# Optimization experiments

Hardware: AMD Instinct MI355X
Metric: run time of the kernel (lower is better)

The kernel has to match this reference:

```python
import jax, jax.numpy as jnp
import numpy as np

N, E = 40000, 640000
IN_DIM, EDGE_DIM, HID, H1 = 5, 11, 128, 4
NEG_SLOPE = 0.2


def _add_self_loops(ei, ea, n):
    # PyG GATConv default: add_self_loops=True, fill_value='mean' for edge_attr
    loop = jnp.arange(n, dtype=ei.dtype)
    ei2 = jnp.concatenate([ei, jnp.stack([loop, loop])], axis=1)
    ea2 = jnp.concatenate([ea, jnp.broadcast_to(ea.mean(0), (n, ea.shape[1]))], axis=0)
    return ei2, ea2


def _gat(x, ei, ea, W, We, a_src, a_dst, a_edge, b, H, C):
    # Single GATConv layer (eval mode, dropout inactive)
    n = x.shape[0]
    xh = (x @ W).reshape(n, H, C)            # [N,H,C]
    eh = (ea @ We).reshape(-1, H, C)         # [E,H,C]
    src, dst = ei[0], ei[1]
    a_s = (xh * a_src).sum(-1)               # [N,H]
    a_d = (xh * a_dst).sum(-1)               # [N,H]
    alpha = jax.nn.leaky_relu(a_s[src] + a_d[dst] + (eh * a_edge).sum(-1), NEG_SLOPE)  # [E,H]
    amax = jax.ops.segment_max(alpha, dst, num_segments=n)
    ex = jnp.exp(alpha - amax[dst])
    den = jax.ops.segment_sum(ex, dst, num_segments=n)
    w = ex / (den[dst] + 1e-16)              # softmax over inbound edges per dst
    out = jax.ops.segment_sum(xh[src] * w[:, :, None], dst, num_segments=n)  # [N,H,C]
    return out.reshape(n, H * C) + b


def setup_inputs() -> dict:
    key = jax.random.key(0)
    ks = jax.random.split(key, 20)
    s = 0.1
    return {
        "x": jax.random.normal(ks[0], (N, IN_DIM), jnp.float32),
        "edge_index": jax.random.randint(ks[1], (2, E), 0, N),
        "edge_attr": jax.random.normal(ks[2], (E, EDGE_DIM), jnp.float32),
        "W1": jax.random.normal(ks[3], (IN_DIM, H1 * HID), jnp.float32) * s,
        "We1": jax.random.normal(ks[4], (EDGE_DIM, H1 * HID), jnp.float32) * s,
        "a_src1": jax.random.normal(ks[5], (H1, HID), jnp.float32) * s,
        "a_dst1": jax.random.normal(ks[6], (H1, HID), jnp.float32) * s,
        "a_edge1": jax.random.normal(ks[7], (H1, HID), jnp.float32) * s,
        "b1": jnp.zeros((H1 * HID,), jnp.float32),
        # layer 2 (512 -> 128, 1 head)
        "W2": jax.random.normal(ks[8], (H1 * HID, HID), jnp.float32) * s,
        "We2": jax.random.normal(ks[9], (EDGE_DIM, HID), jnp.float32) * s,
        "a_src2": jax.random.normal(ks[10], (1, HID), jnp.float32) * s,
        "a_dst2": jax.random.normal(ks[11], (1, HID), jnp.float32) * s,
        "a_edge2": jax.random.normal(ks[12], (1, HID), jnp.float32) * s,
        "b2": jnp.zeros((HID,), jnp.float32),
        # final linear 128 -> 1
        "Wfc": jax.random.normal(ks[13], (HID, 1), jnp.float32) * s,
        "bfc": jnp.zeros((1,), jnp.float32),
    }


def reference(x, edge_index, edge_attr,
              W1, We1, a_src1, a_dst1, a_edge1, b1,
              W2, We2, a_src2, a_dst2, a_edge2, b2,
              Wfc, bfc):
    ei, ea = _add_self_loops(edge_index, edge_attr, x.shape[0])
    h = jax.nn.relu(_gat(x, ei, ea, W1, We1, a_src1, a_dst1, a_edge1, b1, H1, HID))
    h = jax.nn.relu(_gat(h, ei, ea, W2, We2, a_src2, a_dst2, a_edge2, b2, 1, HID))
    return jax.nn.sigmoid(h @ Wfc + bfc)
```

## Files before the change

### kernel.cpp

```cpp
#include <hip/hip_runtime.h>

#define NN   40000
#define EE   640000
#define IND  5
#define ED   11
#define HIDD 128
#define F1   512
#define PSB  2500

typedef unsigned short u16;
typedef unsigned int   u32;
typedef __attribute__((ext_vector_type(8))) short bf16x8;
typedef __attribute__((ext_vector_type(4))) float f32x4;

__device__ __forceinline__ float bf2f(u16 u) { return __uint_as_float(((u32)u) << 16); }
__device__ __forceinline__ u16 f2bf(float f) {
    u32 u = __float_as_uint(f);
    return (u16)((u + 0x7FFFu + ((u >> 16) & 1u)) >> 16);
}

__device__ __forceinline__ float wsum(float v) {
#pragma unroll
    for (int o = 32; o; o >>= 1) v += __shfl_xor(v, o, 64);
    return v;
}
__device__ __forceinline__ float lrelu(float v) { return v > 0.f ? v : 0.2f * v; }



#define SBLK 256
#define SGRID ((NN + SBLK - 1) / SBLK)
#define PREPG (SGRID + 33 + NN / 4)

__global__ void __launch_bounds__(256) k_prep(int* __restrict__ counts,
                                              float* __restrict__ consts,
                                              const float* __restrict__ We1,
                                              const float* __restrict__ ae1,
                                              const float* __restrict__ We2,
                                              const float* __restrict__ ae2,
                                              const float* __restrict__ W2,
                                              u16* __restrict__ bsw,
                                              const float* __restrict__ x,
                                              const float* __restrict__ W1,
                                              const float* __restrict__ as1,
                                              const float* __restrict__ ad1,
                                              float* __restrict__ aS1,
                                              float* __restrict__ aD1) {
    int bid = blockIdx.x, t = threadIdx.x;
    if (bid < SGRID) {
        int i = bid * 256 + t;
        if (i < NN) counts[i] = 0;
        return;
    }
    if (bid == SGRID) {
        if (t < 44) {
            int k = t >> 2, h = t & 3;
            float s = 0.f;
            for (int c = 0; c < HIDD; ++c)
                s += We1[k * F1 + h * HIDD + c] * ae1[h * HIDD + c];
            consts[16 + t] = s;
        }
        if (t >= 48 && t < 48 + ED) {
            int k = t - 48;
            float s = 0.f;
            for (int c = 0; c < HIDD; ++c)
                s += We2[k * HIDD + c] * ae2[c];
            consts[64 + k] = s;
        }
        return;
    }
    if (bid < SGRID + 33) {
        int t2 = (bid - (SGRID + 1)) * 256 + t;
        if (t2 >= 8192) return;
        int lane = t2 & 63, ks = (t2 >> 6) & 15, nt = t2 >> 10;
        int kbase = ks * 32 + (lane >> 4) * 8;
        int n = nt * 16 + (lane & 15);
        size_t dst = (size_t)t2 * 8;
#pragma unroll
        for (int j = 0; j < 8; ++j)
            bsw[dst + j] = f2bf(W2[(size_t)(kbase + j) * HIDD + n]);
        return;
    }
    int n = (bid - (SGRID + 33)) * 4 + (t >> 6);
    int lane = t & 63;
    int c0 = lane * 8, h = lane >> 4;
    const float* xp = x + (size_t)n * IND;
    float x0 = xp[0], x1 = xp[1], x2 = xp[2], x3 = xp[3], x4 = xp[4];
    float p = 0.f, q = 0.f;
#pragma unroll
    for (int j = 0; j < 8; ++j) {
        int c = c0 + j;
        float v = x0 * W1[0 * F1 + c] + x1 * W1[1 * F1 + c] + x2 * W1[2 * F1 + c]
                + x3 * W1[3 * F1 + c] + x4 * W1[4 * F1 + c];
        p += v * as1[c];
        q += v * ad1[c];
    }
#pragma unroll
    for (int o = 1; o <= 8; o <<= 1) {
        p += __shfl_xor(p, o, 64);
        q += __shfl_xor(q, o, 64);
    }
    if ((lane & 15) == 0) {
        aS1[n * 4 + h] = p;
        aD1[n * 4 + h] = q;
    }
}

__global__ void k_count(const int* __restrict__ ei, int* __restrict__ counts,
                        int* __restrict__ rank) {
    int i = blockIdx.x * blockDim.x + threadIdx.x;
    if (i >= EE) return;
    rank[i] = atomicAdd(&counts[ei[EE + i]], 1);
}

__global__ void __launch_bounds__(SBLK) k_scanA(const int* __restrict__ counts,
                                                int* __restrict__ local_ex,
                                                int* __restrict__ bsum) {
    __shared__ int sh[SBLK];
    int t = threadIdx.x;
    int i = blockIdx.x * SBLK + t;
    int v = (i < NN) ? counts[i] : 0;
    sh[t] = v;
    __syncthreads();
    for (int o = 1; o < SBLK; o <<= 1) {
        int u = (t >= o) ? sh[t - o] : 0;
        __syncthreads();
        sh[t] += u;
        __syncthreads();
    }
    if (i < NN) local_ex[i] = sh[t] - v;
    if (t == SBLK - 1) bsum[blockIdx.x] = sh[t];
}

__global__ void __launch_bounds__(SBLK) k_scanC(const int* __restrict__ local_ex,
                                                const int* __restrict__ bsum,
                                                int* __restrict__ row_off) {
    __shared__ int sh[SBLK];
    int t = threadIdx.x, b = blockIdx.x;
    sh[t] = (t < b && t < SGRID) ? bsum[t] : 0;
    __syncthreads();
    for (int o = 128; o; o >>= 1) {
        if (t < o) sh[t] += sh[t + o];
        __syncthreads();
    }
    int boff = sh[0];
    int i = b * SBLK + t;
    if (i < NN) row_off[i] = local_ex[i] + boff;
    if (b == 0 && t == 0) row_off[NN] = EE;
}

__global__ void __launch_bounds__(256) k_build(const float* __restrict__ ea,
                                               const int* __restrict__ ei,
                                               const int* __restrict__ rank,
                                               const int* __restrict__ row_off,
                                               const float* __restrict__ consts,
                                               uint4* __restrict__ rec,
                                               float* __restrict__ psum) {
    __shared__ float sh[4 * ED];
    int i = blockIdx.x * 256 + threadIdx.x;
    int s = ei[i];
    int d = ei[EE + i];
    int pos = row_off[d] + rank[i];
    const float* row = ea + (size_t)i * ED;
    float r[ED];
#pragma unroll
    for (int k = 0; k < ED; ++k) r[k] = row[k];
    float e0 = 0.f, e1 = 0.f, e2 = 0.f, e3 = 0.f, et = 0.f;
#pragma unroll
    for (int k = 0; k < ED; ++k) {
        float a = r[k];
        e0 += a * consts[16 + k * 4 + 0];
        e1 += a * consts[16 + k * 4 + 1];
        e2 += a * consts[16 + k * 4 + 2];
        e3 += a * consts[16 + k * 4 + 3];
        et += a * consts[64 + k];
    }
    uint4 q;
    q.x = (u32)f2bf(e0) | ((u32)f2bf(e1) << 16);
    q.y = (u32)f2bf(e2) | ((u32)f2bf(e3) << 16);
    q.z = (u32)s;
    q.w = __float_as_uint(et);
    rec[pos] = q;
#pragma unroll
    for (int k = 0; k < ED; ++k) r[k] = wsum(r[k]);
    int wv = threadIdx.x >> 6, lane = threadIdx.x & 63;
    if (lane < ED) sh[wv * ED + lane] = r[lane];
    __syncthreads();
    int t = threadIdx.x;
    if (t < ED)
        psum[(size_t)blockIdx.x * ED + t] =
            sh[t] + sh[ED + t] + sh[2 * ED + t] + sh[3 * ED + t];
}

__global__ void __launch_bounds__(256) k_sumred(const float* __restrict__ psum,
                                                float* __restrict__ consts) {
    __shared__ float sh[4 * ED];
    __shared__ float mean[ED];
    int t = threadIdx.x;
    float acc[ED];
#pragma unroll
    for (int k = 0; k < ED; ++k) acc[k] = 0.f;
    for (int w = t; w < PSB; w += 256) {
        const float* p = psum + (size_t)w * ED;
#pragma unroll
        for (int k = 0; k < ED; ++k) acc[k] += p[k];
    }
#pragma unroll
    for (int k = 0; k < ED; ++k) acc[k] = wsum(acc[k]);
    int wv = t >> 6, lane = t & 63;
    if (lane < ED) sh[wv * ED + lane] = acc[lane];
    __syncthreads();
    if (t < ED) {
        float m = (sh[t] + sh[ED + t] + sh[2 * ED + t] + sh[3 * ED + t])
                  * (1.0f / (float)EE);
        mean[t] = m;
        consts[t] = m;
    }
    __syncthreads();
    if (t < 4) {
        float s = 0.f;
        for (int k = 0; k < ED; ++k) s += mean[k] * consts[16 + k * 4 + t];
        consts[80 + t] = s;
    }
    if (t == 8) {
        float s = 0.f;
        for (int k = 0; k < ED; ++k) s += mean[k] * consts[64 + k];
        consts[96] = s;
    }
}

__global__ void __launch_bounds__(256) k_agg1(const int* __restrict__ row_off,
                                              const uint4* __restrict__ rec,
                                              const float* __restrict__ aS1,
                                              const float* __restrict__ aD1,
                                              const float* __restrict__ x,
                                              const float* __restrict__ W1,
                                              const float* __restrict__ b1,
                                              const float* __restrict__ consts,
                                              u16* __restrict__ h1) {
    int n = blockIdx.x * 4 + (threadIdx.x >> 6);
    int t = threadIdx.x & 63;
    int s0 = row_off[n], s1 = row_off[n + 1];
    int h = t & 3;
    float4 adv = *(const float4*)(aD1 + (size_t)n * 4);
    float adh = (h == 0) ? adv.x : (h == 1) ? adv.y : (h == 2) ? adv.z : adv.w;
    float z = 0.f, xa0 = 0.f, xa1 = 0.f, xa2 = 0.f, xa3 = 0.f, xa4 = 0.f;
    for (int i = s0 + (t >> 2); i < s1; i += 16) {
        uint4 q = rec[i];
        u32 w2 = (h & 2) ? q.y : q.x;
        float eh = bf2f((h & 1) ? (u16)(w2 >> 16) : (u16)(w2 & 0xFFFF));
        int s = (int)q.z;
        float a = lrelu(eh + aS1[(size_t)s * 4 + h] + adh);
        float ex = __expf(a);
        z += ex;
        const float* xp = x + (size_t)s * IND;
        xa0 += ex * xp[0]; xa1 += ex * xp[1]; xa2 += ex * xp[2];
        xa3 += ex * xp[3]; xa4 += ex * xp[4];
    }
    if (t < 4) {
        float a = lrelu(consts[80 + h] + aS1[(size_t)n * 4 + h] + adh);
        float ex = __expf(a);
        z += ex;
        const float* xp = x + (size_t)n * IND;
        xa0 += ex * xp[0]; xa1 += ex * xp[1]; xa2 += ex * xp[2];
        xa3 += ex * xp[3]; xa4 += ex * xp[4];
    }
#pragma unroll
    for (int o = 4; o <= 32; o <<= 1) {
        z   += __shfl_xor(z, o, 64);
        xa0 += __shfl_xor(xa0, o, 64); xa1 += __shfl_xor(xa1, o, 64);
        xa2 += __shfl_xor(xa2, o, 64); xa3 += __shfl_xor(xa3, o, 64);
        xa4 += __shfl_xor(xa4, o, 64);
    }
    int ho = t >> 4;
    float zz = __shfl(z, ho);
    float y0 = __shfl(xa0, ho), y1 = __shfl(xa1, ho), y2 = __shfl(xa2, ho);
    float y3 = __shfl(xa3, ho), y4 = __shfl(xa4, ho);
    float ih = 1.f / (zz + 1e-16f);
    int c0 = t * 8;
#pragma unroll
    for (int j = 0; j < 8; ++j) {
        int c = c0 + j;
        float v = (y0 * W1[0 * F1 + c] + y1 * W1[1 * F1 + c] + y2 * W1[2 * F1 + c]
                 + y3 * W1[3 * F1 + c] + y4 * W1[4 * F1 + c]) * ih;
        h1[(size_t)n * F1 + c] = f2bf(fmaxf(v + b1[c], 0.f));
    }
}

__global__ void __launch_bounds__(256, 2) k_gemm2(const u16* __restrict__ h1,
                                                  const u16* __restrict__ bsw,
                                                  const float* __restrict__ as2,
                                                  const float* __restrict__ ad2,
                                                  u16* __restrict__ xh2,
                                                  float* __restrict__ aS2,
                                                  float* __restrict__ aD2) {
    int tid = threadIdx.x;
    int wv = tid >> 6, lane = tid & 63;
    int tile = blockIdx.x * 4 + wv;
    if (tile >= 2500) return;
    int n0 = tile * 16;
    int mrow = lane & 15, quad = lane >> 4;
    const u16* aptr = h1 + (size_t)(n0 + mrow) * F1 + quad * 8;
    const u16* bbase = bsw + lane * 8;
    f32x4 acc[8];
#pragma unroll
    for (int nt = 0; nt < 8; ++nt) acc[nt] = (f32x4){0.f, 0.f, 0.f, 0.f};

    bf16x8 b0[8], b1v[8];
    bf16x8 af0, af1;
    af0 = *(const bf16x8*)(aptr);
#pragma unroll
    for (int nt = 0; nt < 8; ++nt)
        b0[nt] = *(const bf16x8*)(bbase + nt * 8192);
#pragma unroll
    for (int ks = 0; ks < 16; ++ks) {
        if (ks < 15) {
            af1 = *(const bf16x8*)(aptr + (ks + 1) * 32);
#pragma unroll
            for (int nt = 0; nt < 8; ++nt)
                b1v[nt] = *(const bf16x8*)(bbase + nt * 8192 + (ks + 1) * 512);
        }
#pragma unroll
        for (int nt = 0; nt < 8; ++nt)
            acc[nt] = __builtin_amdgcn_mfma_f32_16x16x32_bf16(af0, b0[nt], acc[nt], 0, 0, 0);
        af0 = af1;
#pragma unroll
        for (int nt = 0; nt < 8; ++nt) b0[nt] = b1v[nt];
    }
    float ps[4] = {0.f, 0.f, 0.f, 0.f}, pd[4] = {0.f, 0.f, 0.f, 0.f};
#pragma unroll
    for (int nt = 0; nt < 8; ++nt) {
        int col = nt * 16 + mrow;
        float sa = as2[col], da = ad2[col];
#pragma unroll
        for (int r = 0; r < 4; ++r) {
            float v = acc[nt][r];
            xh2[(size_t)(n0 + quad * 4 + r) * HIDD + col] = f2bf(v);
            ps[r] += v * sa; pd[r] += v * da;
        }
    }
#pragma unroll
    for (int r = 0; r < 4; ++r) {
#pragma unroll
        for (int o = 1; o <= 8; o <<= 1) {
            ps[r] += __shfl_xor(ps[r], o, 64);
            pd[r] += __shfl_xor(pd[r], o, 64);
        }
        if (mrow == 0) {
            aS2[n0 + quad * 4 + r] = ps[r];
            aD2[n0 + quad * 4 + r] = pd[r];
        }
    }
}

__global__ void __launch_bounds__(256) k_agg2(const int* __restrict__ row_off,
                                              const uint4* __restrict__ rec,
                                              const float* __restrict__ aS2,
                                              const float* __restrict__ aD2,
                                              const u16* __restrict__ xh2,
                                              const float* __restrict__ bias2,
                                              const float* __restrict__ Wfc,
                                              const float* __restrict__ bfc,
                                              const float* __restrict__ consts,
                                              float* __restrict__ out) {
    int n = blockIdx.x * 4 + (threadIdx.x >> 6);
    int t = threadIdx.x & 63;
    int s0 = row_off[n], s1 = row_off[n + 1];
    float adn = aD2[n];
    int g = t >> 4, l = t & 15;
    int c0 = l * 8;
    float z = 0.f;
    float acc[8];
#pragma unroll
    for (int j = 0; j < 8; ++j) acc[j] = 0.f;
    for (int i = s0 + g; i < s1; i += 4) {
        uint4 qe = rec[i];
        int s = (int)qe.z;
        float et2 = __uint_as_float(qe.w);
        float ex = __expf(lrelu(aS2[s] + adn + et2));
        z += ex;
        uint4 q = *(const uint4*)(xh2 + (size_t)s * HIDD + c0);
        acc[0] += ex * bf2f((u16)(q.x & 0xFFFF)); acc[1] += ex * bf2f((u16)(q.x >> 16));
        acc[2] += ex * bf2f((u16)(q.y & 0xFFFF)); acc[3] += ex * bf2f((u16)(q.y >> 16));
        acc[4] += ex * bf2f((u16)(q.z & 0xFFFF)); acc[5] += ex * bf2f((u16)(q.z >> 16));
        acc[6] += ex * bf2f((u16)(q.w & 0xFFFF)); acc[7] += ex * bf2f((u16)(q.w >> 16));
    }
    if (g == 0) {
        float ex = __expf(lrelu(aS2[n] + adn + consts[96]));
        z += ex;
        uint4 q = *(const uint4*)(xh2 + (size_t)n * HIDD + c0);
        acc[0] += ex * bf2f((u16)(q.x & 0xFFFF)); acc[1] += ex * bf2f((u16)(q.x >> 16));
        acc[2] += ex * bf2f((u16)(q.y & 0xFFFF)); acc[3] += ex * bf2f((u16)(q.y >> 16));
        acc[4] += ex * bf2f((u16)(q.z & 0xFFFF)); acc[5] += ex * bf2f((u16)(q.z >> 16));
        acc[6] += ex * bf2f((u16)(q.w & 0xFFFF)); acc[7] += ex * bf2f((u16)(q.w >> 16));
    }
#pragma unroll
    for (int o = 16; o <= 32; o <<= 1) {
        z += __shfl_xor(z, o, 64);
#pragma unroll
        for (int j = 0; j < 8; ++j) acc[j] += __shfl_xor(acc[j], o, 64);
    }
    float inv = 1.f / (z + 1e-16f);
    float p = 0.f;
#pragma unroll
    for (int j = 0; j < 8; ++j) {
        float o = fmaxf(acc[j] * inv + bias2[c0 + j], 0.f);
        p += o * Wfc[c0 + j];
    }
#pragma unroll
    for (int o = 1; o <= 8; o <<= 1) p += __shfl_xor(p, o, 64);
    if (t == 0) {
        float logit = p + bfc[0];
        out[n] = 1.f / (1.f + __expf(-logit));
    }
}

extern "C" void kernel_launch(void* const* d_in, const int* in_sizes, int n_in,
                              void* d_out, int out_size, void* d_ws, size_t ws_size,
                              hipStream_t stream) {
    (void)in_sizes; (void)n_in; (void)out_size; (void)ws_size;
    const float* x   = (const float*)d_in[0];
    const int*   ei  = (const int*)d_in[1];
    const float* ea  = (const float*)d_in[2];
    const float* W1  = (const float*)d_in[3];
    const float* We1 = (const float*)d_in[4];
    const float* as1 = (const float*)d_in[5];
    const float* ad1 = (const float*)d_in[6];
    const float* ae1 = (const float*)d_in[7];
    const float* b1  = (const float*)d_in[8];
    const float* W2  = (const float*)d_in[9];
    const float* We2 = (const float*)d_in[10];
    const float* as2 = (const float*)d_in[11];
    const float* ad2 = (const float*)d_in[12];
    const float* ae2 = (const float*)d_in[13];
    const float* b2v = (const float*)d_in[14];
    const float* Wfc = (const float*)d_in[15];
    const float* bfc = (const float*)d_in[16];
    float* out = (float*)d_out;

    char* ws = (char*)d_ws;
    size_t off = 0;
    auto take = [&](size_t nb) {
        size_t r = off;
        off += (nb + 255) & ~(size_t)255;
        return r;
    };
    float* consts = (float*)(ws + take(1024));
    int* row_off  = (int*)(ws + take((size_t)(NN + 1) * 4));
    int* counts   = (int*)(ws + take((size_t)NN * 4));
    int* local_ex = (int*)(ws + take((size_t)NN * 4));
    int* bsum     = (int*)(ws + take(1024));
    int* rank     = (int*)(ws + take((size_t)EE * 4));
    float* psum   = (float*)(ws + take((size_t)PSB * ED * 4));
    uint4* rec    = (uint4*)(ws + take((size_t)EE * 16));
    float* aS1    = (float*)(ws + take((size_t)NN * 16));
    float* aD1    = (float*)(ws + take((size_t)NN * 16));
    float* aS2    = (float*)(ws + take((size_t)NN * 4));
    float* aD2    = (float*)(ws + take((size_t)NN * 4));
    u16* h1       = (u16*)(ws + take((size_t)NN * F1 * 2));
    u16* xh2      = (u16*)(ws + take((size_t)NN * HIDD * 2));
    u16* w2b      = (u16*)(ws + take((size_t)65536 * 2));

    k_prep<<<PREPG, 256, 0, stream>>>(counts, consts, We1, ae1, We2, ae2,
                                      W2, w2b, x, W1, as1, ad1, aS1, aD1);
    k_count<<<EE / 256, 256, 0, stream>>>(ei, counts, rank);
    k_scanA<<<SGRID, SBLK, 0, stream>>>(counts, local_ex, bsum);
    k_scanC<<<SGRID, SBLK, 0, stream>>>(local_ex, bsum, row_off);
    k_build<<<PSB, 256, 0, stream>>>(ea, ei, rank, row_off, consts, rec, psum);
    k_sumred<<<1, 256, 0, stream>>>(psum, consts);
    k_agg1<<<NN / 4, 256, 0, stream>>>(row_off, rec, aS1, aD1, x, W1, b1, consts, h1);
    k_gemm2<<<625, 256, 0, stream>>>(h1, w2b, as2, ad2, xh2, aS2, aD2);
    k_agg2<<<NN / 4, 256, 0, stream>>>(row_off, rec, aS2, aD2, xh2, b2v, Wfc, bfc,
                                       consts, out);
}
```

Baseline: 252.0 us.

## Fuse count, scan and mean-reduction kernels to cut launch count

Folds the edge-degree counting into k_prep, with counters zeroed by a memset. The two-pass scan becomes one kernel in which each block re-sums all preceding counts. The separate mean-reduction kernel is replaced by atomic partial sums plus a last-block-done finalisation inside k_build. This removes several kernel launches and their inter-kernel bubbles, at the cost of redundant prefix reads in the scan and atomic contention on the partial-sum rows.

Result: slower. 364.5 us (+44.6%).

```diff
diff --git a/kernel.cpp b/kernel.cpp
--- a/kernel.cpp
+++ b/kernel.cpp
@@ -7,6 +7,7 @@
 #define HIDD 128
 #define F1   512
 #define PSB  2500
+#define PROWS 64
 
 typedef unsigned short u16;
 typedef unsigned int   u32;
@@ -27,12 +28,13 @@
 __device__ __forceinline__ float lrelu(float v) { return v > 0.f ? v : 0.2f * v; }
 
 
-
 #define SBLK 256
 #define SGRID ((NN + SBLK - 1) / SBLK)
-#define PREPG (SGRID + 33 + NN / 4)
-
-__global__ void __launch_bounds__(256) k_prep(int* __restrict__ counts,
+#define PREPG (PSB + 33 + NN / 4)
+
+__global__ void __launch_bounds__(256) k_prep(const int* __restrict__ ei,
+                                              int* __restrict__ counts,
+                                              int* __restrict__ rank,
                                               float* __restrict__ consts,
                                               const float* __restrict__ We1,
                                               const float* __restrict__ ae1,
@@ -47,12 +49,12 @@
                                               float* __restrict__ aS1,
                                               float* __restrict__ aD1) {
     int bid = blockIdx.x, t = threadIdx.x;
-    if (bid < SGRID) {
+    if (bid < PSB) {
         int i = bid * 256 + t;
-        if (i < NN) counts[i] = 0;
+        rank[i] = atomicAdd(&counts[ei[EE + i]], 1);
         return;
     }
-    if (bid == SGRID) {
+    if (bid == PSB) {
         if (t < 44) {
             int k = t >> 2, h = t & 3;
             float s = 0.f;
@@ -69,8 +71,8 @@
         }
         return;
     }
-    if (bid < SGRID + 33) {
-        int t2 = (bid - (SGRID + 1)) * 256 + t;
+    if (bid < PSB + 33) {
+        int t2 = (bid - (PSB + 1)) * 256 + t;
         if (t2 >= 8192) return;
         int lane = t2 & 63, ks = (t2 >> 6) & 15, nt = t2 >> 10;
         int kbase = ks * 32 + (lane >> 4) * 8;
@@ -81,7 +83,7 @@
             bsw[dst + j] = f2bf(W2[(size_t)(kbase + j) * HIDD + n]);
         return;
     }
-    int n = (bid - (SGRID + 33)) * 4 + (t >> 6);
+    int n = (bid - (PSB + 33)) * 4 + (t >> 6);
     int lane = t & 63;
     int c0 = lane * 8, h = lane >> 4;
     const float* xp = x + (size_t)n * IND;
@@ -106,19 +108,24 @@
     }
 }
 
-__global__ void k_count(const int* __restrict__ ei, int* __restrict__ counts,
-                        int* __restrict__ rank) {
-    int i = blockIdx.x * blockDim.x + threadIdx.x;
-    if (i >= EE) return;
-    rank[i] = atomicAdd(&counts[ei[EE + i]], 1);
-}
-
-__global__ void __launch_bounds__(SBLK) k_scanA(const int* __restrict__ counts,
-                                                int* __restrict__ local_ex,
-                                                int* __restrict__ bsum) {
+__global__ void __launch_bounds__(SBLK) k_scan(const int* __restrict__ counts,
+                                               int* __restrict__ row_off) {
     __shared__ int sh[SBLK];
-    int t = threadIdx.x;
-    int i = blockIdx.x * SBLK + t;
+    __shared__ int s_boff;
+    int t = threadIdx.x, b = blockIdx.x;
+    int acc = 0;
+    for (int i = t; i < b * SBLK; i += SBLK) acc += counts[i];
+    sh[t] = acc;
+    __syncthreads();
+    for (int o = 128; o; o >>= 1) {
+        if (t < o) sh[t] += sh[t + o];
+        __syncthreads();
+    }
+    if (t == 0) s_boff = sh[0];
+    __syncthreads();
+    int boff = s_boff;
+    __syncthreads();
+    int i = b * SBLK + t;
     int v = (i < NN) ? counts[i] : 0;
     sh[t] = v;
     __syncthreads();
@@ -128,24 +135,7 @@
         sh[t] += u;
         __syncthreads();
     }
-    if (i < NN) local_ex[i] = sh[t] - v;
-    if (t == SBLK - 1) bsum[blockIdx.x] = sh[t];
-}
-
-__global__ void __launch_bounds__(SBLK) k_scanC(const int* __restrict__ local_ex,
-                                                const int* __restrict__ bsum,
-                                                int* __restrict__ row_off) {
-    __shared__ int sh[SBLK];
-    int t = threadIdx.x, b = blockIdx.x;
-    sh[t] = (t < b && t < SGRID) ? bsum[t] : 0;
-    __syncthreads();
-    for (int o = 128; o; o >>= 1) {
-        if (t < o) sh[t] += sh[t + o];
-        __syncthreads();
-    }
-    int boff = sh[0];
-    int i = b * SBLK + t;
-    if (i < NN) row_off[i] = local_ex[i] + boff;
+    if (i < NN) row_off[i] = boff + sh[t] - v;
     if (b == 0 && t == 0) row_off[NN] = EE;
 }
 
@@ -153,11 +143,15 @@
                                                const int* __restrict__ ei,
                                                const int* __restrict__ rank,
                                                const int* __restrict__ row_off,
-                                               const float* __restrict__ consts,
+                                               float* __restrict__ consts,
                                                uint4* __restrict__ rec,
-                                               float* __restrict__ psum) {
-    __shared__ float sh[4 * ED];
-    int i = blockIdx.x * 256 + threadIdx.x;
+                                               float* __restrict__ psum,
+                                               int* __restrict__ done) {
+    __shared__ float shf[4 * ED];
+    __shared__ float sh_mean[ED];
+    __shared__ int s_last;
+    int t = threadIdx.x;
+    int i = blockIdx.x * 256 + t;
     int s = ei[i];
     int d = ei[EE + i];
     int pos = row_off[d] + rank[i];
@@ -183,49 +177,35 @@
     rec[pos] = q;
 #pragma unroll
     for (int k = 0; k < ED; ++k) r[k] = wsum(r[k]);
-    int wv = threadIdx.x >> 6, lane = threadIdx.x & 63;
-    if (lane < ED) sh[wv * ED + lane] = r[lane];
-    __syncthreads();
-    int t = threadIdx.x;
+    int wv = t >> 6, lane = t & 63;
+    if (lane < ED) shf[wv * ED + lane] = r[lane];
+    __syncthreads();
     if (t < ED)
-        psum[(size_t)blockIdx.x * ED + t] =
-            sh[t] + sh[ED + t] + sh[2 * ED + t] + sh[3 * ED + t];
-}
-
-__global__ void __launch_bounds__(256) k_sumred(const float* __restrict__ psum,
-                                                float* __restrict__ consts) {
-    __shared__ float sh[4 * ED];
-    __shared__ float mean[ED];
-    int t = threadIdx.x;
-    float acc[ED];
-#pragma unroll
-    for (int k = 0; k < ED; ++k) acc[k] = 0.f;
-    for (int w = t; w < PSB; w += 256) {
-        const float* p = psum + (size_t)w * ED;
-#pragma unroll
-        for (int k = 0; k < ED; ++k) acc[k] += p[k];
-    }
-#pragma unroll
-    for (int k = 0; k < ED; ++k) acc[k] = wsum(acc[k]);
-    int wv = t >> 6, lane = t & 63;
-    if (lane < ED) sh[wv * ED + lane] = acc[lane];
-    __syncthreads();
-    if (t < ED) {
-        float m = (sh[t] + sh[ED + t] + sh[2 * ED + t] + sh[3 * ED + t])
-                  * (1.0f / (float)EE);
-        mean[t] = m;
-        consts[t] = m;
-    }
-    __syncthreads();
-    if (t < 4) {
-        float s = 0.f;
-        for (int k = 0; k < ED; ++k) s += mean[k] * consts[16 + k * 4 + t];
-        consts[80 + t] = s;
-    }
-    if (t == 8) {
-        float s = 0.f;
-        for (int k = 0; k < ED; ++k) s += mean[k] * consts[64 + k];
-        consts[96] = s;
+        atomicAdd(&psum[(blockIdx.x & (PROWS - 1)) * ED + t],
+                  shf[t] + shf[ED + t] + shf[2 * ED + t] + shf[3 * ED + t]);
+    if (t == 0) {
+        __threadfence();
+        s_last = (atomicAdd(done, 1) == PSB - 1) ? 1 : 0;
+    }
+    __syncthreads();
+    if (s_last) {
+        __threadfence();
+        if (t < ED) {
+            float m = 0.f;
+            for (int rr = 0; rr < PROWS; ++rr) m += psum[rr * ED + t];
+            sh_mean[t] = m * (1.0f / (float)EE);
+        }
+        __syncthreads();
+        if (t < 4) {
+            float sv = 0.f;
+            for (int k = 0; k < ED; ++k) sv += sh_mean[k] * consts[16 + k * 4 + t];
+            consts[80 + t] = sv;
+        }
+        if (t == 8) {
+            float sv = 0.f;
+            for (int k = 0; k < ED; ++k) sv += sh_mean[k] * consts[64 + k];
+            consts[96] = sv;
+        }
     }
 }
 
@@ -446,12 +426,12 @@
         return r;
     };
     float* consts = (float*)(ws + take(1024));
+    float* psum   = (float*)(ws + take((size_t)PROWS * ED * 4));
+    int*   done   = (int*)(ws + take(256));
+    int*   counts = (int*)(ws + take((size_t)NN * 4));
+    size_t zbytes = off;
     int* row_off  = (int*)(ws + take((size_t)(NN + 1) * 4));
-    int* counts   = (int*)(ws + take((size_t)NN * 4));
-    int* local_ex = (int*)(ws + take((size_t)NN * 4));
-    int* bsum     = (int*)(ws + take(1024));
     int* rank     = (int*)(ws + take((size_t)EE * 4));
-    float* psum   = (float*)(ws + take((size_t)PSB * ED * 4));
     uint4* rec    = (uint4*)(ws + take((size_t)EE * 16));
     float* aS1    = (float*)(ws + take((size_t)NN * 16));
     float* aD1    = (float*)(ws + take((size_t)NN * 16));
@@ -461,13 +441,11 @@
     u16* xh2      = (u16*)(ws + take((size_t)NN * HIDD * 2));
     u16* w2b      = (u16*)(ws + take((size_t)65536 * 2));
 
-    k_prep<<<PREPG, 256, 0, stream>>>(counts, consts, We1, ae1, We2, ae2,
+    hipMemsetAsync(ws, 0, zbytes, stream);
+    k_prep<<<PREPG, 256, 0, stream>>>(ei, counts, rank, consts, We1, ae1, We2, ae2,
                                       W2, w2b, x, W1, as1, ad1, aS1, aD1);
-    k_count<<<EE / 256, 256, 0, stream>>>(ei, counts, rank);
-    k_scanA<<<SGRID, SBLK, 0, stream>>>(counts, local_ex, bsum);
-    k_scanC<<<SGRID, SBLK, 0, stream>>>(local_ex, bsum, row_off);
-    k_build<<<PSB, 256, 0, stream>>>(ea, ei, rank, row_off, consts, rec, psum);
-    k_sumred<<<1, 256, 0, stream>>>(psum, consts);
+    k_scan<<<SGRID, SBLK, 0, stream>>>(counts, row_off);
+    k_build<<<PSB, 256, 0, stream>>>(ea, ei, rank, row_off, consts, rec, psum, done);
     k_agg1<<<NN / 4, 256, 0, stream>>>(row_off, rec, aS1, aD1, x, W1, b1, consts, h1);
     k_gemm2<<<625, 256, 0, stream>>>(h1, w2b, as2, ad2, xh2, aS2, aD2);
     k_agg2<<<NN / 4, 256, 0, stream>>>(row_off, rec, aS2, aD2, xh2, b2v, Wfc, bfc,
```
